# Kernel optimization log

Measured on AMD Instinct MI355X. Metric: run time of the kernel, lower is better.

Reference implementation:

```python
import jax, jax.numpy as jnp
import numpy as np

N_NODES = 100000
N_EDGES = 1600000
IN_CH, HID_CH, OUT_CH = 512, 128, 128


def gcn_conv(x, src, dst, deg_isqrt, W, b, n_nodes):
    # PyG GCNConv: linear transform, then symmetric-normalized scatter-add
    h = x @ W  # [N, F_out]
    norm = deg_isqrt[src] * deg_isqrt[dst]  # [E+N]
    msg = h[src] * norm[:, None]  # gather + scale
    out = jax.ops.segment_sum(msg, dst, num_segments=n_nodes)
    return out + b


def setup_inputs() -> dict:
    key = jax.random.key(0)
    k1, k2, k3, k4 = jax.random.split(key, 4)
    x = jax.random.normal(k1, (N_NODES, IN_CH), dtype=jnp.float32)
    edge_index = jax.random.randint(k2, (2, N_EDGES), 0, N_NODES, dtype=jnp.int64)
    # Glorot-ish init for weights
    W1 = jax.random.normal(k3, (IN_CH, HID_CH), dtype=jnp.float32) / np.sqrt(IN_CH)
    W2 = jax.random.normal(k4, (HID_CH, OUT_CH), dtype=jnp.float32) / np.sqrt(HID_CH)
    b1 = jnp.zeros((HID_CH,), dtype=jnp.float32)
    b2 = jnp.zeros((OUT_CH,), dtype=jnp.float32)
    return {"x": x, "edge_index": edge_index, "W1": W1, "b1": b1, "W2": W2, "b2": b2}


def reference(x, edge_index, W1, b1, W2, b2):
    n_nodes = x.shape[0]
    # add self-loops (PyG default add_self_loops=True)
    loops = jnp.arange(n_nodes, dtype=edge_index.dtype)
    src = jnp.concatenate([edge_index[0], loops])
    dst = jnp.concatenate([edge_index[1], loops])
    # degree (in-degree over edges incl. self-loops), shared by both layers
    deg = jax.ops.segment_sum(jnp.ones_like(dst, dtype=x.dtype), dst, num_segments=n_nodes)
    deg_isqrt = jax.lax.rsqrt(deg)  # deg >= 1 thanks to self-loops
    h = gcn_conv(x, src, dst, deg_isqrt, W1, b1, n_nodes)
    h = jax.nn.relu(h)
    out = gcn_conv(h, src, dst, deg_isqrt, W2, b2, n_nodes)
    return out
```

## Files before the change

### kernel.cpp

```cpp
#include <hip/hip_runtime.h>
#include <hip/hip_bf16.h>

#define CH 128
#define IN_CH_K 512
#define CHUNK 8192
#define BPAD 5120

typedef short s16x8 __attribute__((ext_vector_type(8)));
typedef float f32x4 __attribute__((ext_vector_type(4)));

__device__ __forceinline__ unsigned int f2bf(float f) {
    unsigned int u = __builtin_bit_cast(unsigned int, f);
    return (u + 0x7fffu + ((u >> 16) & 1u)) >> 16;
}
__device__ __forceinline__ float bf_lo(unsigned int u) {
    return __builtin_bit_cast(float, u << 16);
}
__device__ __forceinline__ float bf_hi(unsigned int u) {
    return __builtin_bit_cast(float, u & 0xFFFF0000u);
}
__device__ __forceinline__ unsigned int relu_pk(unsigned int w) {
    unsigned int keep = (~w) & 0x80008000u;
    unsigned int mask = keep - (keep >> 15);
    return w & mask;
}

__global__ void init_cursor_kernel(int* __restrict__ cursor, int NB) {
    int i = blockIdx.x * blockDim.x + threadIdx.x;
    if (i < NB) cursor[i] = i * BPAD;
}

__global__ void bin_kernel(const int* __restrict__ src, const int* __restrict__ dst,
                           int* __restrict__ cursor, int* __restrict__ binned,
                           int E, int NB) {
    __shared__ int h[512];
    __shared__ int base[512];
    __shared__ int cur[512];
    for (int i = threadIdx.x; i < NB; i += 256) h[i] = 0;
    __syncthreads();
    const int beg = blockIdx.x * CHUNK;
    const int end = min(E, beg + CHUNK);
    for (int e = beg + threadIdx.x; e < end; e += 256)
        atomicAdd(&h[dst[e] >> 8], 1);
    __syncthreads();
    for (int i = threadIdx.x; i < NB; i += 256) {
        cur[i] = 0;
        if (h[i]) base[i] = atomicAdd(&cursor[i], h[i]);
    }
    __syncthreads();
    for (int e = beg + threadIdx.x; e < end; e += 256) {
        int d = dst[e];
        int b = d >> 8;
        int r = atomicAdd(&cur[b], 1);
        int idx = base[b] + r;
        if (idx < (b + 1) * BPAD)
            binned[idx] = src[e] | ((d & 255) << 17);
    }
}

__global__ void csr_bucket_kernel(const int* __restrict__ binned, const int* __restrict__ cursor,
                                  int2* __restrict__ row_range, int* __restrict__ csr_src,
                                  float* __restrict__ dinv, int N) {
    __shared__ int cnt[256];
    __shared__ int off[256];
    __shared__ int cur[256];
    const int k = blockIdx.x;
    const int t = threadIdx.x;
    cnt[t] = 0;
    __syncthreads();
    const int beg = k * BPAD;
    const int end = min(cursor[k], (k + 1) * BPAD);
    for (int e = beg + t; e < end; e += 256)
        atomicAdd(&cnt[binned[e] >> 17], 1);
    __syncthreads();
    int v = cnt[t];
    off[t] = v;
    __syncthreads();
    #pragma unroll
    for (int o = 1; o < 256; o <<= 1) {
        int tv = (t >= o) ? off[t - o] : 0;
        __syncthreads();
        off[t] += tv;
        __syncthreads();
    }
    int ex = off[t] - v;
    int node = k * 256 + t;
    if (node < N) {
        row_range[node] = make_int2(beg + ex, beg + ex + v);
        dinv[node] = rsqrtf((float)(v + 1));
    }
    cur[t] = ex;
    __syncthreads();
    for (int e = beg + t; e < end; e += 256) {
        int p = binned[e];
        int dl = p >> 17;
        int r = atomicAdd(&cur[dl], 1);
        csr_src[beg + r] = p & 0x1FFFF;
    }
}

template<bool PERM>
__global__ void convert_w_kernel(const float* __restrict__ W, uint4* __restrict__ WT, int K) {
    int i = blockIdx.x * blockDim.x + threadIdx.x;
    int ng = K >> 3;
    if (i >= ng * CH) return;
    int g = i >> 7;
    int col = i & 127;
    unsigned int h[8];
    #pragma unroll
    for (int j = 0; j < 8; ++j) {
        int kp = g * 8 + j;
        int k = PERM ? ((kp >> 3) + ((kp & 7) << 4)) : kp;
        h[j] = f2bf(W[(size_t)k * CH + col]);
    }
    uint4 v;
    v.x = h[0] | (h[1] << 16);
    v.y = h[2] | (h[3] << 16);
    v.z = h[4] | (h[5] << 16);
    v.w = h[6] | (h[7] << 16);
    WT[i] = v;
}

__launch_bounds__(256)
__global__ void gemm1_mfma_kernel(const float* __restrict__ A, const uint4* __restrict__ WT,
                                  const float* __restrict__ dinv, unsigned short* __restrict__ C,
                                  int M) {
    const int tid = threadIdx.x;
    const int wid = tid >> 6;
    const int lane = tid & 63;
    const int l15 = lane & 15;
    const int lg = lane >> 4;

    const int block_row = blockIdx.x * 128 + wid * 32;

    f32x4 acc[2][8];
    #pragma unroll
    for (int m = 0; m < 2; ++m)
        #pragma unroll
        for (int n = 0; n < 8; ++n)
            acc[m][n] = (f32x4){0.f, 0.f, 0.f, 0.f};

    int arow0 = block_row + l15;
    int arow1 = block_row + 16 + l15;
    arow0 = (arow0 < M) ? arow0 : (M - 1);
    arow1 = (arow1 < M) ? arow1 : (M - 1);
    const float* aptr0 = A + (size_t)arow0 * IN_CH_K + lg * 8;
    const float* aptr1 = A + (size_t)arow1 * IN_CH_K + lg * 8;

    for (int k0 = 0; k0 < IN_CH_K; k0 += 32) {
        s16x8 afrag[2];
        #pragma unroll
        for (int m = 0; m < 2; ++m) {
            const float* ap = (m == 0 ? aptr0 : aptr1) + k0;
            float4 f0 = *reinterpret_cast<const float4*>(ap);
            float4 f1 = *reinterpret_cast<const float4*>(ap + 4);
            s16x8 a;
            a[0] = (short)f2bf(f0.x); a[1] = (short)f2bf(f0.y);
            a[2] = (short)f2bf(f0.z); a[3] = (short)f2bf(f0.w);
            a[4] = (short)f2bf(f1.x); a[5] = (short)f2bf(f1.y);
            a[6] = (short)f2bf(f1.z); a[7] = (short)f2bf(f1.w);
            afrag[m] = a;
        }
        const int gbase = (k0 >> 3) + lg;
        #pragma unroll
        for (int n = 0; n < 8; ++n) {
            uint4 bv = WT[(size_t)gbase * CH + n * 16 + l15];
            s16x8 b = __builtin_bit_cast(s16x8, bv);
            acc[0][n] = __builtin_amdgcn_mfma_f32_16x16x32_bf16(afrag[0], b, acc[0][n], 0, 0, 0);
            acc[1][n] = __builtin_amdgcn_mfma_f32_16x16x32_bf16(afrag[1], b, acc[1][n], 0, 0, 0);
        }
    }

    #pragma unroll
    for (int m = 0; m < 2; ++m) {
        #pragma unroll
        for (int i = 0; i < 4; ++i) {
            int row = block_row + m * 16 + lg * 4 + i;
            if (row < M) {
                float s = dinv[row];
                uint4 v;
                v.x = f2bf(acc[m][0][i] * s) | (f2bf(acc[m][1][i] * s) << 16);
                v.y = f2bf(acc[m][2][i] * s) | (f2bf(acc[m][3][i] * s) << 16);
                v.z = f2bf(acc[m][4][i] * s) | (f2bf(acc[m][5][i] * s) << 16);
                v.w = f2bf(acc[m][6][i] * s) | (f2bf(acc[m][7][i] * s) << 16);
                *reinterpret_cast<uint4*>(&C[(size_t)row * CH + l15 * 8]) = v;
            }
        }
    }
}

__launch_bounds__(256)
__global__ void gemm2_mfma_kernel(const unsigned short* __restrict__ A, const uint4* __restrict__ WT,
                                  const float* __restrict__ dinv, unsigned short* __restrict__ C,
                                  int M) {
    const int tid = threadIdx.x;
    const int wid = tid >> 6;
    const int lane = tid & 63;
    const int l15 = lane & 15;
    const int lg = lane >> 4;

    const int block_row = blockIdx.x * 128 + wid * 32;

    f32x4 acc[2][8];
    #pragma unroll
    for (int m = 0; m < 2; ++m)
        #pragma unroll
        for (int n = 0; n < 8; ++n)
            acc[m][n] = (f32x4){0.f, 0.f, 0.f, 0.f};

    int arow0 = block_row + l15;
    int arow1 = block_row + 16 + l15;
    arow0 = (arow0 < M) ? arow0 : (M - 1);
    arow1 = (arow1 < M) ? arow1 : (M - 1);
    const uint4* ap0 = reinterpret_cast<const uint4*>(A + (size_t)arow0 * CH);
    const uint4* ap1 = reinterpret_cast<const uint4*>(A + (size_t)arow1 * CH);

    #pragma unroll
    for (int k0 = 0; k0 < CH; k0 += 32) {
        const int fi = (k0 >> 3) + lg;
        uint4 r0 = ap0[fi];
        uint4 r1 = ap1[fi];
        r0.x = relu_pk(r0.x); r0.y = relu_pk(r0.y); r0.z = relu_pk(r0.z); r0.w = relu_pk(r0.w);
        r1.x = relu_pk(r1.x); r1.y = relu_pk(r1.y); r1.z = relu_pk(r1.z); r1.w = relu_pk(r1.w);
        s16x8 a0 = __builtin_bit_cast(s16x8, r0);
        s16x8 a1 = __builtin_bit_cast(s16x8, r1);
        #pragma unroll
        for (int n = 0; n < 8; ++n) {
            uint4 bv = WT[(size_t)fi * CH + n * 16 + l15];
            s16x8 b = __builtin_bit_cast(s16x8, bv);
            acc[0][n] = __builtin_amdgcn_mfma_f32_16x16x32_bf16(a0, b, acc[0][n], 0, 0, 0);
            acc[1][n] = __builtin_amdgcn_mfma_f32_16x16x32_bf16(a1, b, acc[1][n], 0, 0, 0);
        }
    }

    #pragma unroll
    for (int m = 0; m < 2; ++m) {
        #pragma unroll
        for (int i = 0; i < 4; ++i) {
            int row = block_row + m * 16 + lg * 4 + i;
            if (row < M) {
                float s = dinv[row];
                uint4 v;
                v.x = f2bf(acc[m][0][i] * s) | (f2bf(acc[m][1][i] * s) << 16);
                v.y = f2bf(acc[m][2][i] * s) | (f2bf(acc[m][3][i] * s) << 16);
                v.z = f2bf(acc[m][4][i] * s) | (f2bf(acc[m][5][i] * s) << 16);
                v.w = f2bf(acc[m][6][i] * s) | (f2bf(acc[m][7][i] * s) << 16);
                *reinterpret_cast<uint4*>(&C[(size_t)row * CH + l15 * 8]) = v;
            }
        }
    }
}

template<bool OUT_BF16>
__launch_bounds__(256)
__global__ void aggregate_kernel(const unsigned int* __restrict__ g, const int2* __restrict__ row_range,
                                 const int* __restrict__ csr_src, const float* __restrict__ dinv,
                                 const float* __restrict__ bias, void* __restrict__ outp, int N) {
    const int gtid = blockIdx.x * blockDim.x + threadIdx.x;
    const int node = gtid >> 6;
    if (node >= N) return;
    const int lane = threadIdx.x & 63;
    const int cp0 = lane << 1;
    const int cp1 = cp0 | 1;
    const int c0 = (cp0 >> 3) + ((cp0 & 7) << 4);
    const int c1 = (cp1 >> 3) + ((cp1 & 7) << 4);

    unsigned int su = g[(size_t)node * 64 + lane];
    float ax = bf_lo(su);
    float ay = bf_hi(su);

    const int2 rr = row_range[node];
    int j = rr.x;
    const int end = rr.y;
    for (; j + 4 <= end; j += 4) {
        int s0 = __builtin_amdgcn_readfirstlane(csr_src[j]);
        int s1 = __builtin_amdgcn_readfirstlane(csr_src[j + 1]);
        int s2 = __builtin_amdgcn_readfirstlane(csr_src[j + 2]);
        int s3 = __builtin_amdgcn_readfirstlane(csr_src[j + 3]);
        unsigned int u0 = g[(size_t)s0 * 64 + lane];
        unsigned int u1 = g[(size_t)s1 * 64 + lane];
        unsigned int u2 = g[(size_t)s2 * 64 + lane];
        unsigned int u3 = g[(size_t)s3 * 64 + lane];
        ax += (bf_lo(u0) + bf_lo(u1)) + (bf_lo(u2) + bf_lo(u3));
        ay += (bf_hi(u0) + bf_hi(u1)) + (bf_hi(u2) + bf_hi(u3));
    }
    for (; j < end; ++j) {
        int s = __builtin_amdgcn_readfirstlane(csr_src[j]);
        unsigned int u = g[(size_t)s * 64 + lane];
        ax += bf_lo(u);
        ay += bf_hi(u);
    }

    const float di = dinv[node];
    float ox = di * ax + bias[c0];
    float oy = di * ay + bias[c1];
    if (OUT_BF16) {
        ((unsigned int*)outp)[(size_t)node * 64 + lane] = f2bf(ox) | (f2bf(oy) << 16);
    } else {
        float* o = (float*)outp + (size_t)node * CH;
        o[c0] = ox;
        o[c1] = oy;
    }
}

extern "C" void kernel_launch(void* const* d_in, const int* in_sizes, int n_in,
                              void* d_out, int out_size, void* d_ws, size_t ws_size,
                              hipStream_t stream) {
    const float* x  = (const float*)d_in[0];
    const int*   ei = (const int*)d_in[1];
    const float* W1 = (const float*)d_in[2];
    const float* b1 = (const float*)d_in[3];
    const float* W2 = (const float*)d_in[4];
    const float* b2 = (const float*)d_in[5];
    float* out = (float*)d_out;

    const int N = in_sizes[0] / IN_CH_K;
    const int E = in_sizes[1] / 2;
    const int* e_src = ei;
    const int* e_dst = ei + E;

    const int NB = (N + 255) >> 8;
    const int NCHUNK = (E + CHUNK - 1) / CHUNK;

    char* w = (char*)d_ws;
    auto alloc = [&](size_t bytes) {
        char* p = w;
        w += (bytes + 255) & ~(size_t)255;
        return p;
    };
    int*   cursor    = (int*)  alloc((size_t)NB * 4);
    int2*  row_range = (int2*) alloc((size_t)N * 8);
    float* dinv      = (float*)alloc((size_t)N * 4);
    int*   csr_src   = (int*)  alloc((size_t)NB * BPAD * 4);
    uint4* w1t       = (uint4*)alloc((size_t)(IN_CH_K / 8) * CH * 16);
    uint4* w2t       = (uint4*)alloc((size_t)(CH / 8) * CH * 16);
    unsigned short* gbuf = (unsigned short*)alloc((size_t)N * CH * 2);
    unsigned short* abuf = (unsigned short*)alloc((size_t)N * CH * 2);
    int* binned = (int*)gbuf;

    init_cursor_kernel<<<(NB + 255) / 256, 256, 0, stream>>>(cursor, NB);
    bin_kernel<<<NCHUNK, 256, 0, stream>>>(e_src, e_dst, cursor, binned, E, NB);
    csr_bucket_kernel<<<NB, 256, 0, stream>>>(binned, cursor, row_range, csr_src, dinv, N);
    convert_w_kernel<false><<<(IN_CH_K / 8 * CH + 255) / 256, 256, 0, stream>>>(W1, w1t, IN_CH_K);
    convert_w_kernel<true><<<(CH / 8 * CH + 255) / 256, 256, 0, stream>>>(W2, w2t, CH);

    const int gemm_grid = (N + 127) / 128;
    const int agg_grid = (N * 64 + 255) / 256;

    gemm1_mfma_kernel<<<gemm_grid, 256, 0, stream>>>(x, w1t, dinv, gbuf, N);
    aggregate_kernel<true><<<agg_grid, 256, 0, stream>>>((const unsigned int*)gbuf, row_range,
                                                         csr_src, dinv, b1, abuf, N);

    gemm2_mfma_kernel<<<gemm_grid, 256, 0, stream>>>(abuf, w2t, dinv, gbuf, N);
    aggregate_kernel<false><<<agg_grid, 256, 0, stream>>>((const unsigned int*)gbuf, row_range,
                                                          csr_src, dinv, b2, out, N);
}
```

Measured before the change: 315.3 us.

## Vectorize binning loads, use packed bf16 convert, deepen aggregate gather pipeline

Shrinks the binning chunk size and switches the bin and CSR bucket kernels to int4 vector loads. Replaces the manual bf16 rounding with the hardware v_cvt_pk_bf16_f32 instruction in both GEMMs and the aggregation, and unrolls the GEMM1 K loop by two. The aggregate kernel now processes neighbours in groups of eight and prefetches the next group's indices so more gathers are in flight. Risks include misaligned int4 loads on the binned buffer (BPAD is a multiple of 4, so this looks fine), more atomic contention from more bin blocks, and higher register pressure.

Result: faster. 289.0 us (-8.3%).

```diff
diff --git a/kernel.cpp b/kernel.cpp
--- a/kernel.cpp
+++ b/kernel.cpp
@@ -3,7 +3,7 @@
 
 #define CH 128
 #define IN_CH_K 512
-#define CHUNK 8192
+#define CHUNK 2048
 #define BPAD 5120
 
 typedef short s16x8 __attribute__((ext_vector_type(8)));
@@ -12,6 +12,11 @@
 __device__ __forceinline__ unsigned int f2bf(float f) {
     unsigned int u = __builtin_bit_cast(unsigned int, f);
     return (u + 0x7fffu + ((u >> 16) & 1u)) >> 16;
+}
+__device__ __forceinline__ unsigned int pk2bf(float lo, float hi) {
+    unsigned int r;
+    asm("v_cvt_pk_bf16_f32 %0, %1, %2" : "=v"(r) : "v"(lo), "v"(hi));
+    return r;
 }
 __device__ __forceinline__ float bf_lo(unsigned int u) {
     return __builtin_bit_cast(float, u << 16);
@@ -36,25 +41,56 @@
     __shared__ int h[512];
     __shared__ int base[512];
     __shared__ int cur[512];
-    for (int i = threadIdx.x; i < NB; i += 256) h[i] = 0;
-    __syncthreads();
-    const int beg = blockIdx.x * CHUNK;
-    const int end = min(E, beg + CHUNK);
-    for (int e = beg + threadIdx.x; e < end; e += 256)
-        atomicAdd(&h[dst[e] >> 8], 1);
-    __syncthreads();
-    for (int i = threadIdx.x; i < NB; i += 256) {
+    const int tid = threadIdx.x;
+    for (int i = tid; i < NB; i += 256) h[i] = 0;
+    __syncthreads();
+
+    const int E4 = E >> 2;
+    const int beg4 = blockIdx.x * (CHUNK / 4);
+    const int end4 = min(E4, beg4 + CHUNK / 4);
+    const int4* dst4 = reinterpret_cast<const int4*>(dst);
+    const int4* src4 = reinterpret_cast<const int4*>(src);
+    const bool last = (blockIdx.x == gridDim.x - 1);
+
+    for (int e4 = beg4 + tid; e4 < end4; e4 += 256) {
+        int4 d = dst4[e4];
+        atomicAdd(&h[d.x >> 8], 1);
+        atomicAdd(&h[d.y >> 8], 1);
+        atomicAdd(&h[d.z >> 8], 1);
+        atomicAdd(&h[d.w >> 8], 1);
+    }
+    if (last) {
+        for (int e = (E & ~3) + tid; e < E; e += 256)
+            atomicAdd(&h[dst[e] >> 8], 1);
+    }
+    __syncthreads();
+    for (int i = tid; i < NB; i += 256) {
         cur[i] = 0;
         if (h[i]) base[i] = atomicAdd(&cursor[i], h[i]);
     }
     __syncthreads();
-    for (int e = beg + threadIdx.x; e < end; e += 256) {
-        int d = dst[e];
-        int b = d >> 8;
-        int r = atomicAdd(&cur[b], 1);
-        int idx = base[b] + r;
-        if (idx < (b + 1) * BPAD)
-            binned[idx] = src[e] | ((d & 255) << 17);
+
+    for (int e4 = beg4 + tid; e4 < end4; e4 += 256) {
+        int4 d = dst4[e4];
+        int4 s = src4[e4];
+        int b, r, idx;
+        b = d.x >> 8; r = atomicAdd(&cur[b], 1); idx = base[b] + r;
+        if (idx < (b + 1) * BPAD) binned[idx] = s.x | ((d.x & 255) << 17);
+        b = d.y >> 8; r = atomicAdd(&cur[b], 1); idx = base[b] + r;
+        if (idx < (b + 1) * BPAD) binned[idx] = s.y | ((d.y & 255) << 17);
+        b = d.z >> 8; r = atomicAdd(&cur[b], 1); idx = base[b] + r;
+        if (idx < (b + 1) * BPAD) binned[idx] = s.z | ((d.z & 255) << 17);
+        b = d.w >> 8; r = atomicAdd(&cur[b], 1); idx = base[b] + r;
+        if (idx < (b + 1) * BPAD) binned[idx] = s.w | ((d.w & 255) << 17);
+    }
+    if (last) {
+        for (int e = (E & ~3) + tid; e < E; e += 256) {
+            int d = dst[e];
+            int b = d >> 8;
+            int r = atomicAdd(&cur[b], 1);
+            int idx = base[b] + r;
+            if (idx < (b + 1) * BPAD) binned[idx] = src[e] | ((d & 255) << 17);
+        }
     }
 }
 
@@ -70,7 +106,17 @@
     __syncthreads();
     const int beg = k * BPAD;
     const int end = min(cursor[k], (k + 1) * BPAD);
-    for (int e = beg + t; e < end; e += 256)
+    const int nv = (end - beg) & ~3;
+    const int4* b4 = reinterpret_cast<const int4*>(binned + beg);
+
+    for (int q = t; q * 4 < nv; q += 256) {
+        int4 p = b4[q];
+        atomicAdd(&cnt[p.x >> 17], 1);
+        atomicAdd(&cnt[p.y >> 17], 1);
+        atomicAdd(&cnt[p.z >> 17], 1);
+        atomicAdd(&cnt[p.w >> 17], 1);
+    }
+    for (int e = beg + nv + t; e < end; e += 256)
         atomicAdd(&cnt[binned[e] >> 17], 1);
     __syncthreads();
     int v = cnt[t];
@@ -91,7 +137,15 @@
     }
     cur[t] = ex;
     __syncthreads();
-    for (int e = beg + t; e < end; e += 256) {
+    for (int q = t; q * 4 < nv; q += 256) {
+        int4 p = b4[q];
+        int dl, r;
+        dl = p.x >> 17; r = atomicAdd(&cur[dl], 1); csr_src[beg + r] = p.x & 0x1FFFF;
+        dl = p.y >> 17; r = atomicAdd(&cur[dl], 1); csr_src[beg + r] = p.y & 0x1FFFF;
+        dl = p.z >> 17; r = atomicAdd(&cur[dl], 1); csr_src[beg + r] = p.z & 0x1FFFF;
+        dl = p.w >> 17; r = atomicAdd(&cur[dl], 1); csr_src[beg + r] = p.w & 0x1FFFF;
+    }
+    for (int e = beg + nv + t; e < end; e += 256) {
         int p = binned[e];
         int dl = p >> 17;
         int r = atomicAdd(&cur[dl], 1);
@@ -147,6 +201,7 @@
     const float* aptr0 = A + (size_t)arow0 * IN_CH_K + lg * 8;
     const float* aptr1 = A + (size_t)arow1 * IN_CH_K + lg * 8;
 
+    #pragma unroll 2
     for (int k0 = 0; k0 < IN_CH_K; k0 += 32) {
         s16x8 afrag[2];
         #pragma unroll
@@ -154,12 +209,12 @@
             const float* ap = (m == 0 ? aptr0 : aptr1) + k0;
             float4 f0 = *reinterpret_cast<const float4*>(ap);
             float4 f1 = *reinterpret_cast<const float4*>(ap + 4);
-            s16x8 a;
-            a[0] = (short)f2bf(f0.x); a[1] = (short)f2bf(f0.y);
-            a[2] = (short)f2bf(f0.z); a[3] = (short)f2bf(f0.w);
-            a[4] = (short)f2bf(f1.x); a[5] = (short)f2bf(f1.y);
-            a[6] = (short)f2bf(f1.z); a[7] = (short)f2bf(f1.w);
-            afrag[m] = a;
+            uint4 pk;
+            pk.x = pk2bf(f0.x, f0.y);
+            pk.y = pk2bf(f0.z, f0.w);
+            pk.z = pk2bf(f1.x, f1.y);
+            pk.w = pk2bf(f1.z, f1.w);
+            afrag[m] = __builtin_bit_cast(s16x8, pk);
         }
         const int gbase = (k0 >> 3) + lg;
         #pragma unroll
@@ -179,10 +234,10 @@
             if (row < M) {
                 float s = dinv[row];
                 uint4 v;
-                v.x = f2bf(acc[m][0][i] * s) | (f2bf(acc[m][1][i] * s) << 16);
-                v.y = f2bf(acc[m][2][i] * s) | (f2bf(acc[m][3][i] * s) << 16);
-                v.z = f2bf(acc[m][4][i] * s) | (f2bf(acc[m][5][i] * s) << 16);
-                v.w = f2bf(acc[m][6][i] * s) | (f2bf(acc[m][7][i] * s) << 16);
+                v.x = pk2bf(acc[m][0][i] * s, acc[m][1][i] * s);
+                v.y = pk2bf(acc[m][2][i] * s, acc[m][3][i] * s);
+                v.z = pk2bf(acc[m][4][i] * s, acc[m][5][i] * s);
+                v.w = pk2bf(acc[m][6][i] * s, acc[m][7][i] * s);
                 *reinterpret_cast<uint4*>(&C[(size_t)row * CH + l15 * 8]) = v;
             }
         }
@@ -241,16 +296,17 @@
             if (row < M) {
                 float s = dinv[row];
                 uint4 v;
-                v.x = f2bf(acc[m][0][i] * s) | (f2bf(acc[m][1][i] * s) << 16);
-                v.y = f2bf(acc[m][2][i] * s) | (f2bf(acc[m][3][i] * s) << 16);
-                v.z = f2bf(acc[m][4][i] * s) | (f2bf(acc[m][5][i] * s) << 16);
-                v.w = f2bf(acc[m][6][i] * s) | (f2bf(acc[m][7][i] * s) << 16);
+                v.x = pk2bf(acc[m][0][i] * s, acc[m][1][i] * s);
+                v.y = pk2bf(acc[m][2][i] * s, acc[m][3][i] * s);
+                v.z = pk2bf(acc[m][4][i] * s, acc[m][5][i] * s);
+                v.w = pk2bf(acc[m][6][i] * s, acc[m][7][i] * s);
                 *reinterpret_cast<uint4*>(&C[(size_t)row * CH + l15 * 8]) = v;
             }
         }
     }
 }
 
+#define GATHER(cc) g[(size_t)__builtin_amdgcn_readfirstlane(cc) * 64 + lane]
 template<bool OUT_BF16>
 __launch_bounds__(256)
 __global__ void aggregate_kernel(const unsigned int* __restrict__ g, const int2* __restrict__ row_range,
@@ -260,42 +316,61 @@
     const int node = gtid >> 6;
     if (node >= N) return;
     const int lane = threadIdx.x & 63;
+
+    unsigned int su = g[(size_t)node * 64 + lane];
+    const int2 rr = row_range[node];
+    float ax = bf_lo(su);
+    float ay = bf_hi(su);
+
+    int j = rr.x;
+    const int end = rr.y;
+
+    if (j + 8 <= end) {
+        int c0 = csr_src[j], c1 = csr_src[j+1], c2 = csr_src[j+2], c3 = csr_src[j+3];
+        int c4 = csr_src[j+4], c5 = csr_src[j+5], c6 = csr_src[j+6], c7 = csr_src[j+7];
+        j += 8;
+        while (j + 8 <= end) {
+            int n0 = csr_src[j], n1 = csr_src[j+1], n2 = csr_src[j+2], n3 = csr_src[j+3];
+            int n4 = csr_src[j+4], n5 = csr_src[j+5], n6 = csr_src[j+6], n7 = csr_src[j+7];
+            j += 8;
+            unsigned int u0 = GATHER(c0), u1 = GATHER(c1), u2 = GATHER(c2), u3 = GATHER(c3);
+            unsigned int u4 = GATHER(c4), u5 = GATHER(c5), u6 = GATHER(c6), u7 = GATHER(c7);
+            ax += ((bf_lo(u0) + bf_lo(u1)) + (bf_lo(u2) + bf_lo(u3)))
+                + ((bf_lo(u4) + bf_lo(u5)) + (bf_lo(u6) + bf_lo(u7)));
+            ay += ((bf_hi(u0) + bf_hi(u1)) + (bf_hi(u2) + bf_hi(u3)))
+                + ((bf_hi(u4) + bf_hi(u5)) + (bf_hi(u6) + bf_hi(u7)));
+            c0 = n0; c1 = n1; c2 = n2; c3 = n3;
+            c4 = n4; c5 = n5; c6 = n6; c7 = n7;
+        }
+        unsigned int u0 = GATHER(c0), u1 = GATHER(c1), u2 = GATHER(c2), u3 = GATHER(c3);
+        unsigned int u4 = GATHER(c4), u5 = GATHER(c5), u6 = GATHER(c6), u7 = GATHER(c7);
+        ax += ((bf_lo(u0) + bf_lo(u1)) + (bf_lo(u2) + bf_lo(u3)))
+            + ((bf_lo(u4) + bf_lo(u5)) + (bf_lo(u6) + bf_lo(u7)));
+        ay += ((bf_hi(u0) + bf_hi(u1)) + (bf_hi(u2) + bf_hi(u3)))
+            + ((bf_hi(u4) + bf_hi(u5)) + (bf_hi(u6) + bf_hi(u7)));
+    }
+    for (; j + 2 <= end; j += 2) {
+        int c0 = csr_src[j], c1 = csr_src[j+1];
+        unsigned int u0 = GATHER(c0), u1 = GATHER(c1);
+        ax += bf_lo(u0) + bf_lo(u1);
+        ay += bf_hi(u0) + bf_hi(u1);
+    }
+    if (j < end) {
+        int c0 = csr_src[j];
+        unsigned int u0 = GATHER(c0);
+        ax += bf_lo(u0);
+        ay += bf_hi(u0);
+    }
+
     const int cp0 = lane << 1;
     const int cp1 = cp0 | 1;
     const int c0 = (cp0 >> 3) + ((cp0 & 7) << 4);
     const int c1 = (cp1 >> 3) + ((cp1 & 7) << 4);
-
-    unsigned int su = g[(size_t)node * 64 + lane];
-    float ax = bf_lo(su);
-    float ay = bf_hi(su);
-
-    const int2 rr = row_range[node];
-    int j = rr.x;
-    const int end = rr.y;
-    for (; j + 4 <= end; j += 4) {
-        int s0 = __builtin_amdgcn_readfirstlane(csr_src[j]);
-        int s1 = __builtin_amdgcn_readfirstlane(csr_src[j + 1]);
-        int s2 = __builtin_amdgcn_readfirstlane(csr_src[j + 2]);
-        int s3 = __builtin_amdgcn_readfirstlane(csr_src[j + 3]);
-        unsigned int u0 = g[(size_t)s0 * 64 + lane];
-        unsigned int u1 = g[(size_t)s1 * 64 + lane];
-        unsigned int u2 = g[(size_t)s2 * 64 + lane];
-        unsigned int u3 = g[(size_t)s3 * 64 + lane];
-        ax += (bf_lo(u0) + bf_lo(u1)) + (bf_lo(u2) + bf_lo(u3));
-        ay += (bf_hi(u0) + bf_hi(u1)) + (bf_hi(u2) + bf_hi(u3));
-    }
-    for (; j < end; ++j) {
-        int s = __builtin_amdgcn_readfirstlane(csr_src[j]);
-        unsigned int u = g[(size_t)s * 64 + lane];
-        ax += bf_lo(u);
-        ay += bf_hi(u);
-    }
-
     const float di = dinv[node];
     float ox = di * ax + bias[c0];
     float oy = di * ay + bias[c1];
     if (OUT_BF16) {
-        ((unsigned int*)outp)[(size_t)node * 64 + lane] = f2bf(ox) | (f2bf(oy) << 16);
+        ((unsigned int*)outp)[(size_t)node * 64 + lane] = pk2bf(ox, oy);
     } else {
         float* o = (float*)outp + (size_t)node * CH;
         o[c0] = ox;
```
